# Kernel optimization log

Hardware: AMD Instinct MI355X
Metric: run time of the kernel (lower is better)

## Reference

```python
import jax, jax.numpy as jnp
import numpy as np

N_NODES = 100000
N_EDGES = 800000
HID = 128
N_LAYERS = 3
N_GRAPHS = 64
LN_EPS = 1e-5


def setup_inputs() -> dict:
    key = jax.random.key(0)
    ks = jax.random.split(key, 12)
    s = 1.0 / np.sqrt(HID)  # xavier-ish scale
    return {
        "node_features": jax.random.normal(ks[0], (N_NODES, HID), jnp.float32),
        "edge_attr": jax.random.normal(ks[1], (N_EDGES, HID), jnp.float32),
        "in_proj_w": jax.random.normal(ks[2], (HID, HID), jnp.float32) * s,
        "in_proj_b": jnp.zeros((HID,), jnp.float32),
        "gcn_w": jax.random.normal(ks[3], (N_LAYERS, HID, HID), jnp.float32) * s,
        "gcn_ew": jax.random.normal(ks[4], (N_LAYERS, HID, HID), jnp.float32) * s,
        "gcn_b": jnp.zeros((N_LAYERS, HID), jnp.float32),
        "ln_scale": jnp.ones((N_LAYERS, HID), jnp.float32),
        "ln_bias": jnp.zeros((N_LAYERS, HID), jnp.float32),
        "out_proj_w": jax.random.normal(ks[5], (HID, HID), jnp.float32) * s,
        "out_proj_b": jnp.zeros((HID,), jnp.float32),
        "edge_index": jax.random.randint(ks[6], (2, N_EDGES), 0, N_NODES, jnp.int64),
        "batch": jnp.sort(jax.random.randint(ks[7], (N_NODES,), 0, N_GRAPHS, jnp.int64)),
    }


def _layer_norm(x, scale, bias):
    m = jnp.mean(x, axis=-1, keepdims=True)
    v = jnp.mean(jnp.square(x - m), axis=-1, keepdims=True)
    return (x - m) * jax.lax.rsqrt(v + LN_EPS) * scale + bias


def reference(node_features, edge_attr, in_proj_w, in_proj_b, gcn_w, gcn_ew,
              gcn_b, ln_scale, ln_bias, out_proj_w, out_proj_b,
              edge_index, batch):
    src, dst = edge_index[0], edge_index[1]
    x = node_features @ in_proj_w + in_proj_b  # [N, HID]
    for i in range(N_LAYERS):
        residual = x
        h = x @ gcn_w[i]                       # [N, HID]
        ew = edge_attr @ gcn_ew[i]             # [E, HID] edge gate
        msgs = h[src] * ew                     # [E, HID] gather + gate
        agg = jax.ops.segment_sum(msgs, dst, num_segments=N_NODES)  # scatter-add
        h = jax.nn.relu(agg + gcn_b[i])
        # dropout is identity in eval mode
        if i > 0:
            h = h + residual
        x = _layer_norm(h, ln_scale[i], ln_bias[i])
    x = x @ out_proj_w + out_proj_b            # [N, HID]
    # global mean pool per graph
    sums = jax.ops.segment_sum(x, batch, num_segments=N_GRAPHS)
    counts = jax.ops.segment_sum(jnp.ones((N_NODES,), x.dtype), batch,
                                 num_segments=N_GRAPHS)
    return sums / jnp.maximum(counts, 1.0)[:, None]  # [N_GRAPHS, HID]
```

## Files before the change

### kernel.cpp

```cpp
#include <hip/hip_runtime.h>

#define HID 128

typedef __attribute__((ext_vector_type(8))) short bf16x8;
typedef __attribute__((ext_vector_type(4))) float f32x4;
typedef __attribute__((ext_vector_type(4))) unsigned short u16x4;

__device__ __forceinline__ unsigned short f2bf(float f) {
  union { float f; unsigned u; } v; v.f = f;
  return (unsigned short)((v.u + 0x7FFFu + ((v.u >> 16) & 1u)) >> 16);
}
__device__ __forceinline__ float bf2f(unsigned short h) {
  union { unsigned u; float f; } v; v.u = ((unsigned)h) << 16; return v.f;
}
__device__ __forceinline__ float bf2f_lo(unsigned u) {
  union { unsigned u; float f; } v; v.u = u << 16; return v.f;
}
__device__ __forceinline__ float bf2f_hi(unsigned u) {
  union { unsigned u; float f; } v; v.u = u & 0xffff0000u; return v.f;
}


template<bool SRCF32, bool BIAS, bool OUTBF16>
__global__ __launch_bounds__(256, 3) void gemm_node_kernel(
    const void* __restrict__ Xv, const unsigned short* __restrict__ Wt,
    const float* __restrict__ bias, float* __restrict__ Yf,
    unsigned short* __restrict__ Yb, int nrows)
{
  const int tid  = threadIdx.x;
  const int lane = tid & 63;
  const int wave = tid >> 6;
  const int lr = lane & 15;
  const int lg = lane >> 4;
  const long row0 = (long)blockIdx.x * 128 + wave * 32;

  bf16x8 A[2][4];
  #pragma unroll
  for (int rt = 0; rt < 2; ++rt) {
    long R = row0 + rt * 16 + lr;
    if (R >= nrows) R = nrows - 1;
    if (SRCF32) {
      const float* xp = (const float*)Xv + R * HID;
      #pragma unroll
      for (int ks = 0; ks < 4; ++ks) {
        float4 lo = *(const float4*)(xp + ks * 32 + lg * 8);
        float4 hi = *(const float4*)(xp + ks * 32 + lg * 8 + 4);
        bf16x8 a;
        a[0] = (short)f2bf(lo.x); a[1] = (short)f2bf(lo.y);
        a[2] = (short)f2bf(lo.z); a[3] = (short)f2bf(lo.w);
        a[4] = (short)f2bf(hi.x); a[5] = (short)f2bf(hi.y);
        a[6] = (short)f2bf(hi.z); a[7] = (short)f2bf(hi.w);
        A[rt][ks] = a;
      }
    } else {
      const unsigned short* xp = (const unsigned short*)Xv + R * HID;
      #pragma unroll
      for (int ks = 0; ks < 4; ++ks)
        A[rt][ks] = *(const bf16x8*)(xp + ks * 32 + lg * 8);
    }
  }

  f32x4 acc[2][8];
  #pragma unroll
  for (int rt = 0; rt < 2; ++rt)
    #pragma unroll
    for (int ct = 0; ct < 8; ++ct)
      acc[rt][ct] = (f32x4){0.f, 0.f, 0.f, 0.f};

  #pragma unroll
  for (int ks = 0; ks < 4; ++ks) {
    bf16x8 Bf[8];
    #pragma unroll
    for (int ct = 0; ct < 8; ++ct)
      Bf[ct] = *(const bf16x8*)(Wt + (ct * 16 + lr) * HID + ks * 32 + lg * 8);
    #pragma unroll
    for (int rt = 0; rt < 2; ++rt)
      #pragma unroll
      for (int ct = 0; ct < 8; ++ct)
        acc[rt][ct] = __builtin_amdgcn_mfma_f32_16x16x32_bf16(
            A[rt][ks], Bf[ct], acc[rt][ct], 0, 0, 0);
  }

  #pragma unroll
  for (int rt = 0; rt < 2; ++rt) {
    #pragma unroll
    for (int r = 0; r < 4; ++r) {
      long e = row0 + rt * 16 + lg * 4 + r;
      if (e < nrows) {
        if (OUTBF16) {
          bf16x8 o;
          #pragma unroll
          for (int ct = 0; ct < 8; ++ct) {
            float v = acc[rt][ct][r];
            if (BIAS) v += bias[ct * 16 + lr];
            o[ct] = (short)f2bf(v);
          }
          *(bf16x8*)(Yb + e * HID + lr * 8) = o;
        } else {
          #pragma unroll
          for (int ct = 0; ct < 8; ++ct) {
            int col = ct * 16 + lr;
            float v = acc[rt][ct][r];
            if (BIAS) v += bias[col];
            Yf[e * HID + col] = v;
          }
        }
      }
    }
  }
}

__global__ __launch_bounds__(256) void gather_ea_kernel(
    const float* __restrict__ EA, const int* __restrict__ perm,
    unsigned short* __restrict__ EAs, int nE)
{
  long idx = (long)blockIdx.x * 256 + threadIdx.x;
  long slot = idx >> 5;
  if (slot >= nE) return;
  int part = (int)(idx & 31);
  const float* xp = EA + (long)perm[slot] * HID + part * 4;
  float4 v = *(const float4*)xp;
  u16x4 o;
  o[0] = f2bf(v.x); o[1] = f2bf(v.y); o[2] = f2bf(v.z); o[3] = f2bf(v.w);
  *(u16x4*)(EAs + slot * HID + part * 4) = o;
}

__global__ __launch_bounds__(256, 3) void tri_edge_gemm_kernel(
    const unsigned short* __restrict__ EAs,
    const unsigned short* __restrict__ Wt,
    unsigned short* __restrict__ msgs, int nE)
{
  const int tid  = threadIdx.x;
  const int lane = tid & 63;
  const int wave = tid >> 6;
  const int lr = lane & 15;
  const int lg = lane >> 4;
  const long row0 = (long)blockIdx.x * 128 + wave * 32;

  bf16x8 A[2][4];
  #pragma unroll
  for (int rt = 0; rt < 2; ++rt) {
    const unsigned short* xp = EAs + (row0 + rt * 16 + lr) * HID;
    #pragma unroll
    for (int ks = 0; ks < 4; ++ks)
      A[rt][ks] = *(const bf16x8*)(xp + ks * 32 + lg * 8);
  }

  #pragma unroll 1
  for (int w = 0; w < 3; ++w) {
    const unsigned short* Wp = Wt + (size_t)w * 16384;
    unsigned short* Mp = msgs + (size_t)w * nE * HID;

    f32x4 acc[2][8];
    #pragma unroll
    for (int rt = 0; rt < 2; ++rt)
      #pragma unroll
      for (int ct = 0; ct < 8; ++ct)
        acc[rt][ct] = (f32x4){0.f, 0.f, 0.f, 0.f};

    #pragma unroll
    for (int ks = 0; ks < 4; ++ks) {
      bf16x8 Bf[8];
      #pragma unroll
      for (int ct = 0; ct < 8; ++ct)
        Bf[ct] = *(const bf16x8*)(Wp + (ct * 16 + lr) * HID + ks * 32 + lg * 8);
      #pragma unroll
      for (int rt = 0; rt < 2; ++rt)
        #pragma unroll
        for (int ct = 0; ct < 8; ++ct)
          acc[rt][ct] = __builtin_amdgcn_mfma_f32_16x16x32_bf16(
              A[rt][ks], Bf[ct], acc[rt][ct], 0, 0, 0);
    }

    #pragma unroll
    for (int rt = 0; rt < 2; ++rt) {
      #pragma unroll
      for (int r = 0; r < 4; ++r) {
        long e = row0 + rt * 16 + lg * 4 + r;
        bf16x8 o;
        #pragma unroll
        for (int ct = 0; ct < 8; ++ct) o[ct] = (short)f2bf(acc[rt][ct][r]);
        *(bf16x8*)(Mp + e * HID + lr * 8) = o;
      }
    }
  }
}

__global__ __launch_bounds__(256) void seg_ln_kernel(
    const unsigned short* __restrict__ msgs, const unsigned short* __restrict__ Hb,
    const int* __restrict__ ssrc, const int* __restrict__ segend,
    const float* __restrict__ b, const float* __restrict__ lnS,
    const float* __restrict__ lnB, const float* res,
    float* __restrict__ xf, unsigned short* __restrict__ xb)
{
  const int lane = threadIdx.x & 63;
  const int wave = threadIdx.x >> 6;
  const int dbase = blockIdx.x * 32 + wave * 8;
  const int c = lane * 2;

  const float2 bb = *(const float2*)&b[c];
  const float2 sc = *(const float2*)&lnS[c];
  const float2 sb = *(const float2*)&lnB[c];

  int p = (dbase == 0) ? 0 : segend[dbase - 1];
  #pragma unroll 1
  for (int j = 0; j < 8; ++j) {
    const long node = dbase + j;
    const int end = segend[node];
    float a00 = 0.f, a01 = 0.f, a10 = 0.f, a11 = 0.f;
    int q = p;
    for (; q + 1 < end; q += 2) {
      int s0 = ssrc[q];
      int s1 = ssrc[q + 1];
      unsigned m0 = *(const unsigned*)(msgs + (long)q * HID + c);
      unsigned h0 = *(const unsigned*)(Hb + (long)s0 * HID + c);
      unsigned m1 = *(const unsigned*)(msgs + (long)(q + 1) * HID + c);
      unsigned h1 = *(const unsigned*)(Hb + (long)s1 * HID + c);
      a00 += bf2f_lo(m0) * bf2f_lo(h0);
      a01 += bf2f_hi(m0) * bf2f_hi(h0);
      a10 += bf2f_lo(m1) * bf2f_lo(h1);
      a11 += bf2f_hi(m1) * bf2f_hi(h1);
    }
    if (q < end) {
      int s = ssrc[q];
      unsigned m = *(const unsigned*)(msgs + (long)q * HID + c);
      unsigned h = *(const unsigned*)(Hb + (long)s * HID + c);
      a00 += bf2f_lo(m) * bf2f_lo(h);
      a01 += bf2f_hi(m) * bf2f_hi(h);
    }
    p = end;

    float v0 = fmaxf(a00 + a10 + bb.x, 0.f);
    float v1 = fmaxf(a01 + a11 + bb.y, 0.f);
    if (res != nullptr) {
      float2 rr = *(const float2*)&res[node * HID + c];
      v0 += rr.x; v1 += rr.y;
    }
    float s = v0 + v1, qq = v0 * v0 + v1 * v1;
    #pragma unroll
    for (int off = 32; off >= 1; off >>= 1) {
      s  += __shfl_xor(s, off);
      qq += __shfl_xor(qq, off);
    }
    float mean = s * (1.f / 128.f);
    float var = qq * (1.f / 128.f) - mean * mean;
    float rstd = rsqrtf(var + 1e-5f);
    float o0 = (v0 - mean) * rstd * sc.x + sb.x;
    float o1 = (v1 - mean) * rstd * sc.y + sb.y;
    *(float2*)&xf[node * HID + c] = make_float2(o0, o1);
    unsigned pk = (unsigned)f2bf(o0) | ((unsigned)f2bf(o1) << 16);
    *(unsigned*)&xb[node * HID + c] = pk;
  }
}

__global__ __launch_bounds__(256, 3) void gemm_edge_fb_kernel(
    const float* __restrict__ EA, const int* __restrict__ perm,
    const unsigned short* __restrict__ Wt, const unsigned short* __restrict__ Hb,
    const int* __restrict__ ssrc, const int* __restrict__ sdst,
    float* __restrict__ agg, int nE)
{
  const int tid  = threadIdx.x;
  const int lane = tid & 63;
  const int wave = tid >> 6;
  const int lr = lane & 15;
  const int lg = lane >> 4;
  const long row0 = (long)blockIdx.x * 128 + wave * 32;

  bf16x8 A[2][4];
  #pragma unroll
  for (int rt = 0; rt < 2; ++rt) {
    long R = row0 + rt * 16 + lr;
    const float* xp = EA + (long)perm[R] * HID;
    #pragma unroll
    for (int ks = 0; ks < 4; ++ks) {
      float4 lo = *(const float4*)(xp + ks * 32 + lg * 8);
      float4 hi = *(const float4*)(xp + ks * 32 + lg * 8 + 4);
      bf16x8 a;
      a[0] = (short)f2bf(lo.x); a[1] = (short)f2bf(lo.y);
      a[2] = (short)f2bf(lo.z); a[3] = (short)f2bf(lo.w);
      a[4] = (short)f2bf(hi.x); a[5] = (short)f2bf(hi.y);
      a[6] = (short)f2bf(hi.z); a[7] = (short)f2bf(hi.w);
      A[rt][ks] = a;
    }
  }

  f32x4 acc[2][8];
  #pragma unroll
  for (int rt = 0; rt < 2; ++rt)
    #pragma unroll
    for (int ct = 0; ct < 8; ++ct)
      acc[rt][ct] = (f32x4){0.f, 0.f, 0.f, 0.f};

  #pragma unroll
  for (int ks = 0; ks < 4; ++ks) {
    bf16x8 Bf[8];
    #pragma unroll
    for (int ct = 0; ct < 8; ++ct)
      Bf[ct] = *(const bf16x8*)(Wt + (ct * 16 + lr) * HID + ks * 32 + lg * 8);
    #pragma unroll
    for (int rt = 0; rt < 2; ++rt)
      #pragma unroll
      for (int ct = 0; ct < 8; ++ct)
        acc[rt][ct] = __builtin_amdgcn_mfma_f32_16x16x32_bf16(
            A[rt][ks], Bf[ct], acc[rt][ct], 0, 0, 0);
  }

  #pragma unroll
  for (int rt = 0; rt < 2; ++rt) {
    const long base = row0 + rt * 16 + lg * 4;
    int4 sv = *(const int4*)(ssrc + base);
    int4 dv = *(const int4*)(sdst + base);
    bf16x8 hv0 = *(const bf16x8*)(Hb + (long)sv.x * HID + lr * 8);
    bf16x8 hv1 = *(const bf16x8*)(Hb + (long)sv.y * HID + lr * 8);
    bf16x8 hv2 = *(const bf16x8*)(Hb + (long)sv.z * HID + lr * 8);
    bf16x8 hv3 = *(const bf16x8*)(Hb + (long)sv.w * HID + lr * 8);

    float am[8];
    #pragma unroll
    for (int ct = 0; ct < 8; ++ct)
      am[ct] = acc[rt][ct][0] * bf2f((unsigned short)hv0[ct]);
    int dprev = dv.x;
    {
      bool same = (dv.y == dprev);
      if (!same) {
        float* ap = agg + (long)dprev * HID + lr;
        #pragma unroll
        for (int ct = 0; ct < 8; ++ct) atomicAdd(ap + ct * 16, am[ct]);
      }
      #pragma unroll
      for (int ct = 0; ct < 8; ++ct) {
        float m = acc[rt][ct][1] * bf2f((unsigned short)hv1[ct]);
        am[ct] = same ? am[ct] + m : m;
      }
      dprev = dv.y;
    }
    {
      bool same = (dv.z == dprev);
      if (!same) {
        float* ap = agg + (long)dprev * HID + lr;
        #pragma unroll
        for (int ct = 0; ct < 8; ++ct) atomicAdd(ap + ct * 16, am[ct]);
      }
      #pragma unroll
      for (int ct = 0; ct < 8; ++ct) {
        float m = acc[rt][ct][2] * bf2f((unsigned short)hv2[ct]);
        am[ct] = same ? am[ct] + m : m;
      }
      dprev = dv.z;
    }
    {
      bool same = (dv.w == dprev);
      if (!same) {
        float* ap = agg + (long)dprev * HID + lr;
        #pragma unroll
        for (int ct = 0; ct < 8; ++ct) atomicAdd(ap + ct * 16, am[ct]);
      }
      #pragma unroll
      for (int ct = 0; ct < 8; ++ct) {
        float m = acc[rt][ct][3] * bf2f((unsigned short)hv3[ct]);
        am[ct] = same ? am[ct] + m : m;
      }
      dprev = dv.w;
    }
    float* ap = agg + (long)dprev * HID + lr;
    #pragma unroll
    for (int ct = 0; ct < 8; ++ct) atomicAdd(ap + ct * 16, am[ct]);
  }
}

__global__ void hist_kernel(const int* __restrict__ dst, int nE,
                            int* __restrict__ hist)
{
  int i = blockIdx.x * 256 + threadIdx.x;
  if (i < nE) atomicAdd(&hist[dst[i]], 1);
}

__global__ __launch_bounds__(256) void scan1_kernel(
    const int* __restrict__ hist, int n, int* __restrict__ partial)
{
  __shared__ int buf[256];
  int t = threadIdx.x;
  int i = blockIdx.x * 256 + t;
  buf[t] = (i < n) ? hist[i] : 0;
  __syncthreads();
  #pragma unroll
  for (int off = 128; off >= 1; off >>= 1) {
    if (t < off) buf[t] += buf[t + off];
    __syncthreads();
  }
  if (t == 0) partial[blockIdx.x] = buf[0];
}

__global__ __launch_bounds__(512) void scan2_kernel(int* __restrict__ partial,
                                                    int nb)
{
  __shared__ int buf[512];
  int t = threadIdx.x;
  buf[t] = (t < nb) ? partial[t] : 0;
  __syncthreads();
  for (int off = 1; off < 512; off <<= 1) {
    int v = (t >= off) ? buf[t - off] : 0;
    __syncthreads();
    buf[t] += v;
    __syncthreads();
  }
  if (t < nb) partial[t] = (t == 0) ? 0 : buf[t - 1];
}

__global__ __launch_bounds__(256) void scan3_kernel(
    const int* __restrict__ hist, const int* __restrict__ partial,
    int* __restrict__ cursor, int n)
{
  __shared__ int buf[256];
  int t = threadIdx.x;
  int i = blockIdx.x * 256 + t;
  int v = (i < n) ? hist[i] : 0;
  buf[t] = v;
  __syncthreads();
  for (int off = 1; off < 256; off <<= 1) {
    int w = (t >= off) ? buf[t - off] : 0;
    __syncthreads();
    buf[t] += w;
    __syncthreads();
  }
  if (i < n) cursor[i] = partial[blockIdx.x] + buf[t] - v;
}

__global__ void scatter_kernel(const int* __restrict__ src,
                               const int* __restrict__ dst, int nE,
                               int* __restrict__ cursor,
                               int* __restrict__ perm,
                               int* __restrict__ ssrc, int* __restrict__ sdst)
{
  int e = blockIdx.x * 256 + threadIdx.x;
  if (e < nE) {
    int d = dst[e];
    int pos = atomicAdd(&cursor[d], 1);
    perm[pos] = e;
    ssrc[pos] = src[e];
    sdst[pos] = d;
  }
}

__global__ __launch_bounds__(256) void prep_w_kernel(
    const float* __restrict__ ipw, const float* __restrict__ gw,
    const float* __restrict__ gew, const float* __restrict__ opw,
    unsigned short* __restrict__ wt)
{
  int idx = blockIdx.x * 1024 + threadIdx.x * 4;
  #pragma unroll
  for (int t = 0; t < 4; ++t) {
    int i = idx + t;
    int m = i >> 14, r = i & 16383;
    int n = r >> 7, k = r & 127;
    const float* srcm;
    bool kperm;
    if (m == 0)      { srcm = ipw; kperm = false; }
    else if (m <= 3) { srcm = gw  + (size_t)(m - 1) * 16384; kperm = true; }
    else if (m <= 6) { srcm = gew + (size_t)(m - 4) * 16384; kperm = false; }
    else             { srcm = opw; kperm = true; }
    int kk = kperm ? ((k & 7) * 16 + (k >> 3)) : k;
    wt[i] = f2bf(srcm[kk * HID + n]);
  }
}

__global__ void prep_params_kernel(const float* __restrict__ gb,
                                   const float* __restrict__ lns,
                                   const float* __restrict__ lnb,
                                   float* __restrict__ bp,
                                   float* __restrict__ lsp,
                                   float* __restrict__ lbp)
{
  int idx = threadIdx.x + blockIdx.x * 128;
  if (idx < 384) {
    int i = idx >> 7, p = idx & 127;
    int c = (p & 7) * 16 + (p >> 3);
    bp[idx]  = gb[i * 128 + c];
    lsp[idx] = lns[i * 128 + c];
    lbp[idx] = lnb[i * 128 + c];
  }
}

__global__ __launch_bounds__(256) void ln_nat_kernel(
    const float* __restrict__ agg, const float* __restrict__ b,
    const float* res, const float* __restrict__ lnS,
    const float* __restrict__ lnB, float* xf, unsigned short* __restrict__ xb,
    int n)
{
  const int wave = threadIdx.x >> 6;
  const int lane = threadIdx.x & 63;
  const long node = (long)blockIdx.x * 4 + wave;
  if (node >= n) return;

  float2 v = *(const float2*)&agg[node * HID + lane * 2];
  float2 bb = *(const float2*)&b[lane * 2];
  v.x += bb.x; v.y += bb.y;
  v.x = fmaxf(v.x, 0.f); v.y = fmaxf(v.y, 0.f);
  if (res != nullptr) {
    float2 rr = *(const float2*)&res[node * HID + lane * 2];
    v.x += rr.x; v.y += rr.y;
  }
  float s = v.x + v.y;
  #pragma unroll
  for (int off = 32; off >= 1; off >>= 1) s += __shfl_xor(s, off);
  float mean = s * (1.f / 128.f);
  float dx = v.x - mean, dy = v.y - mean;
  float q = dx * dx + dy * dy;
  #pragma unroll
  for (int off = 32; off >= 1; off >>= 1) q += __shfl_xor(q, off);
  float rstd = rsqrtf(q * (1.f / 128.f) + 1e-5f);
  float2 sc = *(const float2*)&lnS[lane * 2];
  float2 sb = *(const float2*)&lnB[lane * 2];
  float ox = dx * rstd * sc.x + sb.x;
  float oy = dy * rstd * sc.y + sb.y;
  *(float2*)&xf[node * HID + lane * 2] = make_float2(ox, oy);
  int c0 = lane * 2, c1 = lane * 2 + 1;
  xb[node * HID + ((c0 & 15) * 8 + (c0 >> 4))] = f2bf(ox);
  xb[node * HID + ((c1 & 15) * 8 + (c1 >> 4))] = f2bf(oy);
}

__global__ void graph_count_kernel(const int* __restrict__ batch, int n,
                                   int nG, int* __restrict__ counts)
{
  int g = threadIdx.x;
  if (g >= nG) return;
  int lo0 = 0, hi0 = n;
  while (lo0 < hi0) { int mid = (lo0 + hi0) >> 1; if (batch[mid] < g) lo0 = mid + 1; else hi0 = mid; }
  int lo1 = lo0, hi1 = n;
  while (lo1 < hi1) { int mid = (lo1 + hi1) >> 1; if (batch[mid] < g + 1) lo1 = mid + 1; else hi1 = mid; }
  counts[g] = lo1 - lo0;
}

__global__ __launch_bounds__(128) void pool_kernel(
    const float* __restrict__ X, const int* __restrict__ batch, int n,
    float* __restrict__ sums)
{
  const int col = threadIdx.x;
  long n0 = (long)blockIdx.x * 64;
  long n1 = n0 + 64; if (n1 > n) n1 = n;
  if (n0 >= n) return;
  float s = 0.f;
  int g = batch[n0];
  for (long i = n0; i < n1; ++i) {
    int gi = batch[i];
    if (gi != g) {
      atomicAdd(&sums[g * HID + col], s);
      s = 0.f;
      g = gi;
    }
    s += X[i * HID + col];
  }
  atomicAdd(&sums[g * HID + col], s);
}

__global__ void finalize_kernel(const float* __restrict__ sums,
                                const int* __restrict__ counts,
                                float* __restrict__ out, int total)
{
  int i = blockIdx.x * 256 + threadIdx.x;
  if (i < total) {
    int g = i >> 7;
    float c = (float)counts[g];
    out[i] = sums[i] / fmaxf(c, 1.f);
  }
}

extern "C" void kernel_launch(void* const* d_in, const int* in_sizes, int n_in,
                              void* d_out, int out_size, void* d_ws, size_t ws_size,
                              hipStream_t stream)
{
  const float* nf    = (const float*)d_in[0];
  const float* ea    = (const float*)d_in[1];
  const float* ipw   = (const float*)d_in[2];
  const float* ipb   = (const float*)d_in[3];
  const float* gw    = (const float*)d_in[4];
  const float* gew   = (const float*)d_in[5];
  const float* gb    = (const float*)d_in[6];
  const float* lns   = (const float*)d_in[7];
  const float* lnb   = (const float*)d_in[8];
  const float* opw   = (const float*)d_in[9];
  const float* opb   = (const float*)d_in[10];
  const int*   ei    = (const int*)d_in[11];
  const int*   batch = (const int*)d_in[12];
  float* out = (float*)d_out;

  const int N = 100000;
  const int E = 800000;
  const int G = 64;
  const int* srcI = ei;
  const int* dstI = ei + E;

  char* ws = (char*)d_ws;
  const size_t nodeF = (size_t)N * HID * sizeof(float);
  const size_t nodeB = (size_t)N * HID * sizeof(unsigned short);
  size_t off = 0;
  float*          xf   = (float*)(ws + off); off += nodeF;
  float*          agg  = (float*)(ws + off); off += nodeF;
  unsigned short* xb   = (unsigned short*)(ws + off); off += nodeB;
  unsigned short* hb   = (unsigned short*)(ws + off); off += nodeB;
  unsigned short* wt   = (unsigned short*)(ws + off); off += 8 * 16384 * 2;
  float*          bp   = (float*)(ws + off); off += 384 * 4;
  float*          lsp  = (float*)(ws + off); off += 384 * 4;
  float*          lbp  = (float*)(ws + off); off += 384 * 4;
  int*            perm = (int*)(ws + off); off += (size_t)E * 4;
  int*            ssrc = (int*)(ws + off); off += (size_t)E * 4;
  int*            sdst = (int*)(ws + off); off += (size_t)E * 4;
  int*            hist = (int*)(ws + off); off += (size_t)N * 4;
  int*            curs = (int*)(ws + off); off += (size_t)N * 4;
  int*            part = (int*)(ws + off); off += 512 * 4;
  float*          sums = (float*)(ws + off); off += (size_t)G * HID * 4;
  int*            cnts = (int*)(ws + off); off += G * 4;
  unsigned short* eas  = (unsigned short*)(ws + off);
  off += (size_t)E * HID * sizeof(unsigned short);
  unsigned short* msgs = (unsigned short*)(ws + off);
  off += 3 * (size_t)E * HID * sizeof(unsigned short);
  const bool hoisted = (ws_size >= off);

  dim3 blk(256);
  const int nBlkN = (N + 127) / 128;
  const int nBlkE = E / 128;
  const int nBins = (N + 255) / 256;

  prep_w_kernel<<<128, blk, 0, stream>>>(ipw, gw, gew, opw, wt);
  prep_params_kernel<<<3, dim3(128), 0, stream>>>(gb, lns, lnb, bp, lsp, lbp);

  hipMemsetAsync(hist, 0, (size_t)N * 4, stream);
  hist_kernel<<<(E + 255) / 256, blk, 0, stream>>>(dstI, E, hist);
  scan1_kernel<<<nBins, blk, 0, stream>>>(hist, N, part);
  scan2_kernel<<<1, dim3(512), 0, stream>>>(part, nBins);
  scan3_kernel<<<nBins, blk, 0, stream>>>(hist, part, curs, N);
  scatter_kernel<<<(E + 255) / 256, blk, 0, stream>>>(srcI, dstI, E, curs,
                                                      perm, ssrc, sdst);

  if (hoisted) {
    gather_ea_kernel<<<(int)(((long)E * 32 + 255) / 256), blk, 0, stream>>>(
        ea, perm, eas, E);
    tri_edge_gemm_kernel<<<nBlkE, blk, 0, stream>>>(
        eas, wt + (size_t)4 * 16384, msgs, E);
  }

  gemm_node_kernel<true, true, true><<<nBlkN, blk, 0, stream>>>(
      nf, wt, ipb, nullptr, xb, N);

  for (int i = 0; i < 3; ++i) {
    gemm_node_kernel<false, false, true><<<nBlkN, blk, 0, stream>>>(
        xb, wt + (size_t)(1 + i) * 16384, nullptr, nullptr, hb, N);
    if (hoisted) {
      seg_ln_kernel<<<N / 32, blk, 0, stream>>>(
          msgs + (size_t)i * E * HID, hb, ssrc, curs,
          bp + i * HID, lsp + i * HID, lbp + i * HID,
          (i > 0) ? xf : nullptr, xf, xb);
    } else {
      hipMemsetAsync(agg, 0, nodeF, stream);
      gemm_edge_fb_kernel<<<nBlkE, blk, 0, stream>>>(
          ea, perm, wt + (size_t)(4 + i) * 16384, hb, ssrc, sdst, agg, E);
      ln_nat_kernel<<<(N + 3) / 4, blk, 0, stream>>>(
          agg, gb + i * HID, (i > 0) ? xf : nullptr, lns + i * HID,
          lnb + i * HID, xf, xb, N);
    }
  }

  gemm_node_kernel<false, true, false><<<nBlkN, blk, 0, stream>>>(
      xb, wt + (size_t)7 * 16384, opb, agg, nullptr, N);

  graph_count_kernel<<<1, dim3(64), 0, stream>>>(batch, N, G, cnts);
  hipMemsetAsync(sums, 0, (size_t)G * HID * 4, stream);
  pool_kernel<<<(N + 63) / 64, dim3(128), 0, stream>>>(agg, batch, N, sums);
  finalize_kernel<<<(G * HID + 255) / 256, blk, 0, stream>>>(
      sums, cnts, out, G * HID);
}
```

Baseline: 1.078 ms.

## Fuse edge-attr gather into edge GEMM and keep residual in bf16

The permuted edge-attribute gather and bf16 conversion now happen inside the tri edge GEMM's A-fragment load, so the separate gather kernel and its intermediate bf16 buffer go away. The seg_ln kernel reads the residual from the bf16 node buffer in place and no longer writes the fp32 copy, which cuts memory traffic. The residual is now bf16-rounded, which slightly lowers accuracy. The GEMM also does uncoalesced fp32 row loads.

```diff
diff --git a/kernel.cpp b/kernel.cpp
--- a/kernel.cpp
+++ b/kernel.cpp
@@ -110,23 +110,8 @@
   }
 }
 
-__global__ __launch_bounds__(256) void gather_ea_kernel(
+__global__ __launch_bounds__(256, 3) void tri_edge_gemm_kernel(
     const float* __restrict__ EA, const int* __restrict__ perm,
-    unsigned short* __restrict__ EAs, int nE)
-{
-  long idx = (long)blockIdx.x * 256 + threadIdx.x;
-  long slot = idx >> 5;
-  if (slot >= nE) return;
-  int part = (int)(idx & 31);
-  const float* xp = EA + (long)perm[slot] * HID + part * 4;
-  float4 v = *(const float4*)xp;
-  u16x4 o;
-  o[0] = f2bf(v.x); o[1] = f2bf(v.y); o[2] = f2bf(v.z); o[3] = f2bf(v.w);
-  *(u16x4*)(EAs + slot * HID + part * 4) = o;
-}
-
-__global__ __launch_bounds__(256, 3) void tri_edge_gemm_kernel(
-    const unsigned short* __restrict__ EAs,
     const unsigned short* __restrict__ Wt,
     unsigned short* __restrict__ msgs, int nE)
 {
@@ -140,10 +125,19 @@
   bf16x8 A[2][4];
   #pragma unroll
   for (int rt = 0; rt < 2; ++rt) {
-    const unsigned short* xp = EAs + (row0 + rt * 16 + lr) * HID;
-    #pragma unroll
-    for (int ks = 0; ks < 4; ++ks)
-      A[rt][ks] = *(const bf16x8*)(xp + ks * 32 + lg * 8);
+    long R = row0 + rt * 16 + lr;
+    const float* xp = EA + (long)perm[R] * HID;
+    #pragma unroll
+    for (int ks = 0; ks < 4; ++ks) {
+      float4 lo = *(const float4*)(xp + ks * 32 + lg * 8);
+      float4 hi = *(const float4*)(xp + ks * 32 + lg * 8 + 4);
+      bf16x8 a;
+      a[0] = (short)f2bf(lo.x); a[1] = (short)f2bf(lo.y);
+      a[2] = (short)f2bf(lo.z); a[3] = (short)f2bf(lo.w);
+      a[4] = (short)f2bf(hi.x); a[5] = (short)f2bf(hi.y);
+      a[6] = (short)f2bf(hi.z); a[7] = (short)f2bf(hi.w);
+      A[rt][ks] = a;
+    }
   }
 
   #pragma unroll 1
@@ -190,8 +184,8 @@
     const unsigned short* __restrict__ msgs, const unsigned short* __restrict__ Hb,
     const int* __restrict__ ssrc, const int* __restrict__ segend,
     const float* __restrict__ b, const float* __restrict__ lnS,
-    const float* __restrict__ lnB, const float* res,
-    float* __restrict__ xf, unsigned short* __restrict__ xb)
+    const float* __restrict__ lnB, int useRes,
+    unsigned short* __restrict__ xb)
 {
   const int lane = threadIdx.x & 63;
   const int wave = threadIdx.x >> 6;
@@ -232,9 +226,10 @@
 
     float v0 = fmaxf(a00 + a10 + bb.x, 0.f);
     float v1 = fmaxf(a01 + a11 + bb.y, 0.f);
-    if (res != nullptr) {
-      float2 rr = *(const float2*)&res[node * HID + c];
-      v0 += rr.x; v1 += rr.y;
+    if (useRes) {
+      unsigned rr = *(const unsigned*)(xb + node * HID + c);
+      v0 += bf2f_lo(rr);
+      v1 += bf2f_hi(rr);
     }
     float s = v0 + v1, qq = v0 * v0 + v1 * v1;
     #pragma unroll
@@ -247,7 +242,6 @@
     float rstd = rsqrtf(var + 1e-5f);
     float o0 = (v0 - mean) * rstd * sc.x + sb.x;
     float o1 = (v1 - mean) * rstd * sc.y + sb.y;
-    *(float2*)&xf[node * HID + c] = make_float2(o0, o1);
     unsigned pk = (unsigned)f2bf(o0) | ((unsigned)f2bf(o1) << 16);
     *(unsigned*)&xb[node * HID + c] = pk;
   }
@@ -610,8 +604,6 @@
   int*            part = (int*)(ws + off); off += 512 * 4;
   float*          sums = (float*)(ws + off); off += (size_t)G * HID * 4;
   int*            cnts = (int*)(ws + off); off += G * 4;
-  unsigned short* eas  = (unsigned short*)(ws + off);
-  off += (size_t)E * HID * sizeof(unsigned short);
   unsigned short* msgs = (unsigned short*)(ws + off);
   off += 3 * (size_t)E * HID * sizeof(unsigned short);
   const bool hoisted = (ws_size >= off);
@@ -633,10 +625,8 @@
                                                       perm, ssrc, sdst);
 
   if (hoisted) {
-    gather_ea_kernel<<<(int)(((long)E * 32 + 255) / 256), blk, 0, stream>>>(
-        ea, perm, eas, E);
     tri_edge_gemm_kernel<<<nBlkE, blk, 0, stream>>>(
-        eas, wt + (size_t)4 * 16384, msgs, E);
+        ea, perm, wt + (size_t)4 * 16384, msgs, E);
   }
 
   gemm_node_kernel<true, true, true><<<nBlkN, blk, 0, stream>>>(
@@ -649,7 +639,7 @@
       seg_ln_kernel<<<N / 32, blk, 0, stream>>>(
           msgs + (size_t)i * E * HID, hb, ssrc, curs,
           bp + i * HID, lsp + i * HID, lbp + i * HID,
-          (i > 0) ? xf : nullptr, xf, xb);
+          (i > 0) ? 1 : 0, xb);
     } else {
       hipMemsetAsync(agg, 0, nodeF, stream);
       gemm_edge_fb_kernel<<<nBlkE, blk, 0, stream>>>(
```

Result: faster. 964.5 us (-10.6%).
